# Performance work log

Hardware: AMD Instinct MI355X
Metric: run time of the kernel (lower is better)

## Reference

```python
import jax, jax.numpy as jnp
import numpy as np

NUM_CONN = 8

def _ein_reduce(f):
    # Einstein t-norm fold over last axis: T(a,b) = ab / (2 - (a+b-ab))
    acc = f[..., 0]
    for i in range(1, f.shape[-1]):
        b = f[..., i]
        ab = acc * b
        acc = ab / (2.0 - (acc + b - ab))
    return acc

def _coein_reduce(f):
    # Einstein t-conorm fold over last axis: S(a,b) = (a+b) / (1 + ab)
    acc = f[..., 0]
    for i in range(1, f.shape[-1]):
        b = f[..., i]
        acc = (acc + b) / (1.0 + acc * b)
    return acc

def _ddlg_layer(x, w, idx, is_train):
    # x: [B, in], idx: [out, C] int, w: [out, 4]
    feats = x[:, idx]                      # [B, out, C] gather
    ops = jnp.stack([
        jnp.min(feats, axis=-1),
        jnp.max(feats, axis=-1),
        _ein_reduce(feats),
        _coein_reduce(feats),
    ], axis=-1)                            # [B, out, 4]
    if is_train:
        prob = jax.nn.softmax(w, axis=-1)  # [out, 4]
    else:
        prob = jax.nn.one_hot(jnp.argmax(w, axis=-1), 4, dtype=x.dtype)
    return jnp.einsum('bof,of->bo', ops, prob)

def setup_inputs() -> dict:
    key = jax.random.key(0)
    ks = jax.random.split(key, 6)
    sizes = [4096, 2048, 1024, 2048, 4096]
    x = jax.random.uniform(ks[0], (4096, sizes[0]), dtype=jnp.float32)
    ws = [jax.random.normal(ks[1 + i], (sizes[i + 1], 4), dtype=jnp.float32) for i in range(4)]
    rng = np.random.default_rng(0)
    idxs = []
    for i in range(4):
        # randperm-without-replacement per output neuron
        perm = np.argsort(rng.random((sizes[i + 1], sizes[i])), axis=-1)[:, :NUM_CONN]
        idxs.append(jnp.asarray(perm, dtype=jnp.int32))
    return {
        'x': x,
        'w0': ws[0], 'w1': ws[1], 'w2': ws[2], 'w3': ws[3],
        'idx0': idxs[0], 'idx1': idxs[1], 'idx2': idxs[2], 'idx3': idxs[3],
        'is_train': 1,
    }

def reference(x, w0, w1, w2, w3, idx0, idx1, idx2, idx3, is_train):
    h = _ddlg_layer(x, w0, idx0, is_train)
    h = _ddlg_layer(h, w1, idx1, is_train)
    h = _ddlg_layer(h, w2, idx2, is_train)
    h = _ddlg_layer(h, w3, idx3, is_train)
    return h
```

## Files before the change

kernel.cpp:

```cpp
#include <hip/hip_runtime.h>


#define BATCH 4096

typedef _Float16 h4 __attribute__((ext_vector_type(4)));

__device__ __forceinline__ float fastrcp(float x) { return __builtin_amdgcn_rcpf(x); }
__device__ __forceinline__ _Float16 hrcp(_Float16 x) {
#if __has_builtin(__builtin_amdgcn_rcph)
    return __builtin_amdgcn_rcph(x);
#else
    return (_Float16)__builtin_amdgcn_rcpf((float)x);
#endif
}
__device__ __forceinline__ h4 splat(_Float16 s) { h4 v = {s, s, s, s}; return v; }

__global__ __launch_bounds__(256) void prep_k(const float* __restrict__ w0,
                                              const float* __restrict__ w1,
                                              const float* __restrict__ w2,
                                              const float* __restrict__ w3,
                                              const int* __restrict__ is_train,
                                              h4* __restrict__ probsH) {
    const int g = blockIdx.x * 256 + threadIdx.x;
    const float* w; int o;
    if (g < 2048)      { w = w0; o = g; }
    else if (g < 3072) { w = w1; o = g - 2048; }
    else if (g < 5120) { w = w2; o = g - 3072; }
    else               { w = w3; o = g - 5120; }
    float wv[4];
#pragma unroll
    for (int c = 0; c < 4; ++c) wv[c] = w[(o << 2) + c];
    float p[4];
    if (*is_train) {
        float m = fmaxf(fmaxf(wv[0], wv[1]), fmaxf(wv[2], wv[3]));
        float s = 0.0f;
#pragma unroll
        for (int c = 0; c < 4; ++c) { p[c] = __expf(wv[c] - m); s += p[c]; }
        float inv = fastrcp(s);
#pragma unroll
        for (int c = 0; c < 4; ++c) p[c] *= inv;
    } else {
        int a = 0; float best = wv[0];
#pragma unroll
        for (int c = 1; c < 4; ++c) if (wv[c] > best) { best = wv[c]; a = c; }
#pragma unroll
        for (int c = 0; c < 4; ++c) p[c] = (c == a) ? 1.0f : 0.0f;
    }
    probsH[g] = h4{(_Float16)p[0], (_Float16)p[1], (_Float16)p[2], (_Float16)p[3]};
}

struct Chain { h4 mn, mx, De, Ne, Nc, Dc; };

__device__ __forceinline__ void chain_init(Chain& C, h4 v, h4 one, h4 two) {
    C.mn = v; C.mx = v; C.De = v;
    C.Ne = two - v; C.Nc = one + v; C.Dc = one - v;
}
__device__ __forceinline__ void chain_step(Chain& C, h4 v, h4 two) {
    C.mn = __builtin_elementwise_min(C.mn, v);
    C.mx = __builtin_elementwise_max(C.mx, v);
    C.De *= v;
    C.Ne *= (two - v);
    C.Nc += C.Nc * v;
    C.Dc -= C.Dc * v;
}
__device__ __forceinline__ h4 finale(const Chain& C, h4 P) {
    h4 s1 = C.Ne + C.De;
    h4 s2 = C.Nc + C.Dc;
    h4 d1 = C.Nc - C.Dc;
    h4 ss = s1 * s2;
    h4 r;
#pragma unroll
    for (int e = 0; e < 4; ++e) r[e] = hrcp(ss[e]);
    h4 t1 = (C.De + C.De) * s2;
    h4 t2 = d1 * s1;
    h4 num = splat(P[2]) * t1 + splat(P[3]) * t2;
    return splat(P[0]) * C.mn + splat(P[1]) * C.mx + num * r;
}

__device__ __forceinline__ h4 gate1(const h4* __restrict__ rows,
                                    const int4* __restrict__ idx,
                                    const h4* __restrict__ probs, int o) {
    const int4 i0 = idx[o * 2], i1 = idx[o * 2 + 1];
    const h4 P = probs[o];
    h4 A[8];
    A[0] = rows[i0.x]; A[1] = rows[i0.y]; A[2] = rows[i0.z]; A[3] = rows[i0.w];
    A[4] = rows[i1.x]; A[5] = rows[i1.y]; A[6] = rows[i1.z]; A[7] = rows[i1.w];
    const h4 one = splat((_Float16)1.0f), two = splat((_Float16)2.0f);
    Chain C; chain_init(C, A[0], one, two);
#pragma unroll
    for (int c = 1; c < 8; ++c) chain_step(C, A[c], two);
    return finale(C, P);
}

__device__ __forceinline__ void gate2(const h4* __restrict__ rows,
                                      const int4* __restrict__ idx,
                                      const h4* __restrict__ probs,
                                      int o0, h4& ra, h4& rb) {
    const int4 a0 = idx[o0 * 2],     a1 = idx[o0 * 2 + 1];
    const int4 b0 = idx[o0 * 2 + 2], b1 = idx[o0 * 2 + 3];
    const h4 PA = probs[o0], PB = probs[o0 + 1];
    h4 A[8], B[8];
    A[0] = rows[a0.x]; A[1] = rows[a0.y]; A[2] = rows[a0.z]; A[3] = rows[a0.w];
    A[4] = rows[a1.x]; A[5] = rows[a1.y]; A[6] = rows[a1.z]; A[7] = rows[a1.w];
    B[0] = rows[b0.x]; B[1] = rows[b0.y]; B[2] = rows[b0.z]; B[3] = rows[b0.w];
    B[4] = rows[b1.x]; B[5] = rows[b1.y]; B[6] = rows[b1.z]; B[7] = rows[b1.w];
    const h4 one = splat((_Float16)1.0f), two = splat((_Float16)2.0f);
    Chain CA, CB;
    chain_init(CA, A[0], one, two);
    chain_init(CB, B[0], one, two);
#pragma unroll
    for (int c = 1; c < 8; ++c) {
        chain_step(CA, A[c], two);
        chain_step(CB, B[c], two);
    }
    ra = finale(CA, PA);
    rb = finale(CB, PB);
}

struct alignas(16) H4x2 { h4 a, b; };

__global__ __launch_bounds__(1024, 8) void ddlg_fused(const float* __restrict__ x,
                                                      const h4* __restrict__ probsH,
                                                      const int4* __restrict__ idx0,
                                                      const int4* __restrict__ idx1,
                                                      const int4* __restrict__ idx2,
                                                      const int4* __restrict__ idx3,
                                                      float* __restrict__ out) {
    __shared__ __align__(16) _Float16 lds[24576];
    const int t  = threadIdx.x;
    const int b0 = blockIdx.x << 2;

    const h4* xl  = (const h4*)lds;
    const h4* h0v = (const h4*)(lds + 16384);
    const h4* h1v = (const h4*)lds;
    const h4* h2v = (const h4*)(lds + 16384);

#pragma unroll
    for (int c = 0; c < 4; ++c) {
        const int j = (c << 10) + t;
        const float v0 = x[(size_t)(b0 + 0) * 4096 + j];
        const float v1 = x[(size_t)(b0 + 1) * 4096 + j];
        const float v2 = x[(size_t)(b0 + 2) * 4096 + j];
        const float v3 = x[(size_t)(b0 + 3) * 4096 + j];
        h4 hv;
        hv[0] = (_Float16)v0; hv[1] = (_Float16)v1;
        hv[2] = (_Float16)v2; hv[3] = (_Float16)v3;
        *(h4*)(lds + (j << 2)) = hv;
    }
    __syncthreads();

    {
        h4 ra, rb;
        gate2(xl, idx0, probsH, 2 * t, ra, rb);
        *(H4x2*)(lds + 16384 + (t << 3)) = H4x2{ra, rb};
    }
    __syncthreads();

    {
        h4 r = gate1(h0v, idx1, probsH + 2048, t);
        *(h4*)(lds + (t << 2)) = r;
    }
    __syncthreads();

    {
        h4 ra, rb;
        gate2(h1v, idx2, probsH + 3072, 2 * t, ra, rb);
        *(H4x2*)(lds + 16384 + (t << 3)) = H4x2{ra, rb};
    }
    __syncthreads();

    {
        h4 r0, r1, r2, r3;
        gate2(h2v, idx3, probsH + 5120, 4 * t,     r0, r1);
        gate2(h2v, idx3, probsH + 5120, 4 * t + 2, r2, r3);
#pragma unroll
        for (int b = 0; b < 4; ++b) {
            float4 o4 = make_float4((float)r0[b], (float)r1[b],
                                    (float)r2[b], (float)r3[b]);
            *(float4*)(out + (size_t)(b0 + b) * 4096 + (t << 2)) = o4;
        }
    }
}

extern "C" void kernel_launch(void* const* d_in, const int* in_sizes, int n_in,
                              void* d_out, int out_size, void* d_ws, size_t ws_size,
                              hipStream_t stream) {
    const float* x        = (const float*)d_in[0];
    const float* w0       = (const float*)d_in[1];
    const float* w1       = (const float*)d_in[2];
    const float* w2       = (const float*)d_in[3];
    const float* w3       = (const float*)d_in[4];
    const int4*  idx0     = (const int4*)d_in[5];
    const int4*  idx1     = (const int4*)d_in[6];
    const int4*  idx2     = (const int4*)d_in[7];
    const int4*  idx3     = (const int4*)d_in[8];
    const int*   is_train = (const int*)d_in[9];
    float*       out      = (float*)d_out;

    h4* probsH = (h4*)d_ws;

    prep_k<<<36, 256, 0, stream>>>(w0, w1, w2, w3, is_train, probsH);
    ddlg_fused<<<1024, 1024, 0, stream>>>(x, probsH, idx0, idx1, idx2, idx3, out);
}
```

Measured before the change: 164.2 us.

## Process eight batch rows per block with 16-byte LDS gathers

Each block now handles 8 batch rows instead of 4, storing activations as 8 packed halves (uint4) per feature in LDS. One gathered 16-byte LDS read now serves 8 batch elements, halving index and probability loads per output and amortising gather address work. The cost is twice the LDS per block (96 KB), fewer resident blocks per CU (launch bound lowered to 4), more live registers per thread, and half as many blocks in the grid.

```diff
diff --git a/kernel.cpp b/kernel.cpp
--- a/kernel.cpp
+++ b/kernel.cpp
@@ -3,6 +3,7 @@
 
 #define BATCH 4096
 
+typedef _Float16 h2 __attribute__((ext_vector_type(2)));
 typedef _Float16 h4 __attribute__((ext_vector_type(4)));
 
 __device__ __forceinline__ float fastrcp(float x) { return __builtin_amdgcn_rcpf(x); }
@@ -13,7 +14,7 @@
     return (_Float16)__builtin_amdgcn_rcpf((float)x);
 #endif
 }
-__device__ __forceinline__ h4 splat(_Float16 s) { h4 v = {s, s, s, s}; return v; }
+__device__ __forceinline__ h2 splat2(_Float16 s) { h2 v = {s, s}; return v; }
 
 __global__ __launch_bounds__(256) void prep_k(const float* __restrict__ w0,
                                               const float* __restrict__ w1,
@@ -49,134 +50,145 @@
     probsH[g] = h4{(_Float16)p[0], (_Float16)p[1], (_Float16)p[2], (_Float16)p[3]};
 }
 
-struct Chain { h4 mn, mx, De, Ne, Nc, Dc; };
-
-__device__ __forceinline__ void chain_init(Chain& C, h4 v, h4 one, h4 two) {
-    C.mn = v; C.mx = v; C.De = v;
-    C.Ne = two - v; C.Nc = one + v; C.Dc = one - v;
-}
-__device__ __forceinline__ void chain_step(Chain& C, h4 v, h4 two) {
-    C.mn = __builtin_elementwise_min(C.mn, v);
-    C.mx = __builtin_elementwise_max(C.mx, v);
-    C.De *= v;
-    C.Ne *= (two - v);
-    C.Nc += C.Nc * v;
-    C.Dc -= C.Dc * v;
-}
-__device__ __forceinline__ h4 finale(const Chain& C, h4 P) {
-    h4 s1 = C.Ne + C.De;
-    h4 s2 = C.Nc + C.Dc;
-    h4 d1 = C.Nc - C.Dc;
-    h4 ss = s1 * s2;
-    h4 r;
-#pragma unroll
-    for (int e = 0; e < 4; ++e) r[e] = hrcp(ss[e]);
-    h4 t1 = (C.De + C.De) * s2;
-    h4 t2 = d1 * s1;
-    h4 num = splat(P[2]) * t1 + splat(P[3]) * t2;
-    return splat(P[0]) * C.mn + splat(P[1]) * C.mx + num * r;
-}
-
-__device__ __forceinline__ h4 gate1(const h4* __restrict__ rows,
-                                    const int4* __restrict__ idx,
-                                    const h4* __restrict__ probs, int o) {
+struct Raw8 { h2 q[4]; };
+
+__device__ __forceinline__ Raw8 row_at(const uint4* __restrict__ rows, int i) {
+    const uint4 v = rows[i];
+    Raw8 r;
+    r.q[0] = __builtin_bit_cast(h2, v.x);
+    r.q[1] = __builtin_bit_cast(h2, v.y);
+    r.q[2] = __builtin_bit_cast(h2, v.z);
+    r.q[3] = __builtin_bit_cast(h2, v.w);
+    return r;
+}
+__device__ __forceinline__ uint4 raw_bits(Raw8 r) {
+    return uint4{__builtin_bit_cast(unsigned, r.q[0]), __builtin_bit_cast(unsigned, r.q[1]),
+                 __builtin_bit_cast(unsigned, r.q[2]), __builtin_bit_cast(unsigned, r.q[3])};
+}
+
+struct Chain8 { h2 mn[4], mx[4], De[4], Ne[4], Nc[4], Dc[4]; };
+
+__device__ __forceinline__ void cinit(Chain8& C, Raw8 v) {
+    const h2 one = splat2((_Float16)1.0f), two = splat2((_Float16)2.0f);
+#pragma unroll
+    for (int q = 0; q < 4; ++q) {
+        C.mn[q] = v.q[q]; C.mx[q] = v.q[q]; C.De[q] = v.q[q];
+        C.Ne[q] = two - v.q[q];
+        C.Nc[q] = one + v.q[q];
+        C.Dc[q] = one - v.q[q];
+    }
+}
+__device__ __forceinline__ void cstep(Chain8& C, Raw8 v) {
+    const h2 two = splat2((_Float16)2.0f);
+#pragma unroll
+    for (int q = 0; q < 4; ++q) {
+        C.mn[q] = __builtin_elementwise_min(C.mn[q], v.q[q]);
+        C.mx[q] = __builtin_elementwise_max(C.mx[q], v.q[q]);
+        C.De[q] *= v.q[q];
+        C.Ne[q] *= (two - v.q[q]);
+        C.Nc[q] += C.Nc[q] * v.q[q];
+        C.Dc[q] -= C.Dc[q] * v.q[q];
+    }
+}
+__device__ __forceinline__ Raw8 finale(const Chain8& C, h4 P) {
+    const h2 P0 = splat2(P[0]), P1 = splat2(P[1]);
+    const h2 P2 = splat2(P[2]), P3 = splat2(P[3]);
+    Raw8 res;
+#pragma unroll
+    for (int q = 0; q < 4; ++q) {
+        h2 s1 = C.Ne[q] + C.De[q];
+        h2 s2 = C.Nc[q] + C.Dc[q];
+        h2 d1 = C.Nc[q] - C.Dc[q];
+        h2 ss = s1 * s2;
+        h2 r  = {hrcp(ss[0]), hrcp(ss[1])};
+        h2 t1 = (C.De[q] + C.De[q]) * s2;
+        h2 t2 = d1 * s1;
+        h2 num = P2 * t1 + P3 * t2;
+        res.q[q] = P0 * C.mn[q] + P1 * C.mx[q] + num * r;
+    }
+    return res;
+}
+
+__device__ __forceinline__ Raw8 gate8(const uint4* __restrict__ rows,
+                                      const int4* __restrict__ idx,
+                                      const h4* __restrict__ probs, int o) {
     const int4 i0 = idx[o * 2], i1 = idx[o * 2 + 1];
     const h4 P = probs[o];
-    h4 A[8];
-    A[0] = rows[i0.x]; A[1] = rows[i0.y]; A[2] = rows[i0.z]; A[3] = rows[i0.w];
-    A[4] = rows[i1.x]; A[5] = rows[i1.y]; A[6] = rows[i1.z]; A[7] = rows[i1.w];
-    const h4 one = splat((_Float16)1.0f), two = splat((_Float16)2.0f);
-    Chain C; chain_init(C, A[0], one, two);
-#pragma unroll
-    for (int c = 1; c < 8; ++c) chain_step(C, A[c], two);
+    Raw8 A[8];
+    A[0] = row_at(rows, i0.x); A[1] = row_at(rows, i0.y);
+    A[2] = row_at(rows, i0.z); A[3] = row_at(rows, i0.w);
+    A[4] = row_at(rows, i1.x); A[5] = row_at(rows, i1.y);
+    A[6] = row_at(rows, i1.z); A[7] = row_at(rows, i1.w);
+    Chain8 C; cinit(C, A[0]);
+#pragma unroll
+    for (int c = 1; c < 8; ++c) cstep(C, A[c]);
     return finale(C, P);
 }
 
-__device__ __forceinline__ void gate2(const h4* __restrict__ rows,
-                                      const int4* __restrict__ idx,
-                                      const h4* __restrict__ probs,
-                                      int o0, h4& ra, h4& rb) {
-    const int4 a0 = idx[o0 * 2],     a1 = idx[o0 * 2 + 1];
-    const int4 b0 = idx[o0 * 2 + 2], b1 = idx[o0 * 2 + 3];
-    const h4 PA = probs[o0], PB = probs[o0 + 1];
-    h4 A[8], B[8];
-    A[0] = rows[a0.x]; A[1] = rows[a0.y]; A[2] = rows[a0.z]; A[3] = rows[a0.w];
-    A[4] = rows[a1.x]; A[5] = rows[a1.y]; A[6] = rows[a1.z]; A[7] = rows[a1.w];
-    B[0] = rows[b0.x]; B[1] = rows[b0.y]; B[2] = rows[b0.z]; B[3] = rows[b0.w];
-    B[4] = rows[b1.x]; B[5] = rows[b1.y]; B[6] = rows[b1.z]; B[7] = rows[b1.w];
-    const h4 one = splat((_Float16)1.0f), two = splat((_Float16)2.0f);
-    Chain CA, CB;
-    chain_init(CA, A[0], one, two);
-    chain_init(CB, B[0], one, two);
-#pragma unroll
-    for (int c = 1; c < 8; ++c) {
-        chain_step(CA, A[c], two);
-        chain_step(CB, B[c], two);
-    }
-    ra = finale(CA, PA);
-    rb = finale(CB, PB);
-}
-
-struct alignas(16) H4x2 { h4 a, b; };
-
-__global__ __launch_bounds__(1024, 8) void ddlg_fused(const float* __restrict__ x,
+__global__ __launch_bounds__(1024, 4) void ddlg_fused(const float* __restrict__ x,
                                                       const h4* __restrict__ probsH,
                                                       const int4* __restrict__ idx0,
                                                       const int4* __restrict__ idx1,
                                                       const int4* __restrict__ idx2,
                                                       const int4* __restrict__ idx3,
                                                       float* __restrict__ out) {
-    __shared__ __align__(16) _Float16 lds[24576];
+    __shared__ __align__(16) _Float16 lds[49152];
     const int t  = threadIdx.x;
-    const int b0 = blockIdx.x << 2;
-
-    const h4* xl  = (const h4*)lds;
-    const h4* h0v = (const h4*)(lds + 16384);
-    const h4* h1v = (const h4*)lds;
-    const h4* h2v = (const h4*)(lds + 16384);
+    const int b0 = blockIdx.x << 3;
+
+    const uint4* xv  = (const uint4*)lds;
+    const uint4* h0v = (const uint4*)(lds + 32768);
+    const uint4* h1v = (const uint4*)lds;
+    const uint4* h2v = (const uint4*)(lds + 32768);
 
 #pragma unroll
     for (int c = 0; c < 4; ++c) {
         const int j = (c << 10) + t;
-        const float v0 = x[(size_t)(b0 + 0) * 4096 + j];
-        const float v1 = x[(size_t)(b0 + 1) * 4096 + j];
-        const float v2 = x[(size_t)(b0 + 2) * 4096 + j];
-        const float v3 = x[(size_t)(b0 + 3) * 4096 + j];
-        h4 hv;
-        hv[0] = (_Float16)v0; hv[1] = (_Float16)v1;
-        hv[2] = (_Float16)v2; hv[3] = (_Float16)v3;
-        *(h4*)(lds + (j << 2)) = hv;
-    }
-    __syncthreads();
-
-    {
-        h4 ra, rb;
-        gate2(xl, idx0, probsH, 2 * t, ra, rb);
-        *(H4x2*)(lds + 16384 + (t << 3)) = H4x2{ra, rb};
-    }
-    __syncthreads();
-
-    {
-        h4 r = gate1(h0v, idx1, probsH + 2048, t);
-        *(h4*)(lds + (t << 2)) = r;
-    }
-    __syncthreads();
-
-    {
-        h4 ra, rb;
-        gate2(h1v, idx2, probsH + 3072, 2 * t, ra, rb);
-        *(H4x2*)(lds + 16384 + (t << 3)) = H4x2{ra, rb};
-    }
-    __syncthreads();
-
-    {
-        h4 r0, r1, r2, r3;
-        gate2(h2v, idx3, probsH + 5120, 4 * t,     r0, r1);
-        gate2(h2v, idx3, probsH + 5120, 4 * t + 2, r2, r3);
-#pragma unroll
-        for (int b = 0; b < 4; ++b) {
-            float4 o4 = make_float4((float)r0[b], (float)r1[b],
-                                    (float)r2[b], (float)r3[b]);
+        h2 p[4];
+#pragma unroll
+        for (int qq = 0; qq < 4; ++qq) {
+            const float va = x[(size_t)(b0 + 2 * qq + 0) * 4096 + j];
+            const float vb = x[(size_t)(b0 + 2 * qq + 1) * 4096 + j];
+            p[qq] = h2{(_Float16)va, (_Float16)vb};
+        }
+        uint4 hv = {__builtin_bit_cast(unsigned, p[0]), __builtin_bit_cast(unsigned, p[1]),
+                    __builtin_bit_cast(unsigned, p[2]), __builtin_bit_cast(unsigned, p[3])};
+        *(uint4*)(lds + (j << 3)) = hv;
+    }
+    __syncthreads();
+
+    {
+        Raw8 ra = gate8(xv, idx0, probsH, 2 * t);
+        Raw8 rb = gate8(xv, idx0, probsH, 2 * t + 1);
+        *(uint4*)(lds + 32768 + (t << 4))     = raw_bits(ra);
+        *(uint4*)(lds + 32768 + (t << 4) + 8) = raw_bits(rb);
+    }
+    __syncthreads();
+
+    {
+        Raw8 r = gate8(h0v, idx1, probsH + 2048, t);
+        *(uint4*)(lds + (t << 3)) = raw_bits(r);
+    }
+    __syncthreads();
+
+    {
+        Raw8 ra = gate8(h1v, idx2, probsH + 3072, 2 * t);
+        Raw8 rb = gate8(h1v, idx2, probsH + 3072, 2 * t + 1);
+        *(uint4*)(lds + 32768 + (t << 4))     = raw_bits(ra);
+        *(uint4*)(lds + 32768 + (t << 4) + 8) = raw_bits(rb);
+    }
+    __syncthreads();
+
+    {
+        Raw8 r0 = gate8(h2v, idx3, probsH + 5120, 4 * t);
+        Raw8 r1 = gate8(h2v, idx3, probsH + 5120, 4 * t + 1);
+        Raw8 r2 = gate8(h2v, idx3, probsH + 5120, 4 * t + 2);
+        Raw8 r3 = gate8(h2v, idx3, probsH + 5120, 4 * t + 3);
+#pragma unroll
+        for (int b = 0; b < 8; ++b) {
+            const int q = b >> 1, e = b & 1;
+            float4 o4 = make_float4((float)r0.q[q][e], (float)r1.q[q][e],
+                                    (float)r2.q[q][e], (float)r3.q[q][e]);
             *(float4*)(out + (size_t)(b0 + b) * 4096 + (t << 2)) = o4;
         }
     }
@@ -200,5 +212,5 @@
     h4* probsH = (h4*)d_ws;
 
     prep_k<<<36, 256, 0, stream>>>(w0, w1, w2, w3, is_train, probsH);
-    ddlg_fused<<<1024, 1024, 0, stream>>>(x, probsH, idx0, idx1, idx2, idx3, out);
-}
+    ddlg_fused<<<512, 1024, 0, stream>>>(x, probsH, idx0, idx1, idx2, idx3, out);
+}
```

Measured after the change: 170.8 us. 4.0% more time.

## Process two batch rows per block with 512 threads and packed half2

Applied to the files above, without the earlier changes.

Each block now handles 2 batch rows instead of 4, using 512 threads and 24KB of LDS instead of 1024 threads and 48KB. Activations are stored as packed half2 words and each thread loops over several output neurons per layer. The aim is higher occupancy and smaller blocks with shorter barrier stalls. In exchange, the index and probability loads are amortised over half as many batch rows, and the final output is written as scalar floats instead of float4.

```diff
diff --git a/kernel.cpp b/kernel.cpp
--- a/kernel.cpp
+++ b/kernel.cpp
@@ -1,8 +1,7 @@
 #include <hip/hip_runtime.h>
 
 
-#define BATCH 4096
-
+typedef _Float16 h2 __attribute__((ext_vector_type(2)));
 typedef _Float16 h4 __attribute__((ext_vector_type(4)));
 
 __device__ __forceinline__ float fastrcp(float x) { return __builtin_amdgcn_rcpf(x); }
@@ -13,7 +12,11 @@
     return (_Float16)__builtin_amdgcn_rcpf((float)x);
 #endif
 }
-__device__ __forceinline__ h4 splat(_Float16 s) { h4 v = {s, s, s, s}; return v; }
+__device__ __forceinline__ h2 splat2(_Float16 s) { h2 v = {s, s}; return v; }
+__device__ __forceinline__ unsigned packh2(float a, float b) {
+    h2 v = {(_Float16)a, (_Float16)b};
+    return __builtin_bit_cast(unsigned, v);
+}
 
 __global__ __launch_bounds__(256) void prep_k(const float* __restrict__ w0,
                                               const float* __restrict__ w1,
@@ -49,13 +52,18 @@
     probsH[g] = h4{(_Float16)p[0], (_Float16)p[1], (_Float16)p[2], (_Float16)p[3]};
 }
 
-struct Chain { h4 mn, mx, De, Ne, Nc, Dc; };
+struct Chain { h2 mn, mx, De, Ne, Nc, Dc; };
 
-__device__ __forceinline__ void chain_init(Chain& C, h4 v, h4 one, h4 two) {
+__device__ __forceinline__ h2 row_at(const unsigned* __restrict__ rows, int i) {
+    return __builtin_bit_cast(h2, rows[i]);
+}
+__device__ __forceinline__ void cinit(Chain& C, h2 v) {
+    const h2 one = splat2((_Float16)1.0f), two = splat2((_Float16)2.0f);
     C.mn = v; C.mx = v; C.De = v;
     C.Ne = two - v; C.Nc = one + v; C.Dc = one - v;
 }
-__device__ __forceinline__ void chain_step(Chain& C, h4 v, h4 two) {
+__device__ __forceinline__ void cstep(Chain& C, h2 v) {
+    const h2 two = splat2((_Float16)2.0f);
     C.mn = __builtin_elementwise_min(C.mn, v);
     C.mx = __builtin_elementwise_max(C.mx, v);
     C.De *= v;
@@ -63,122 +71,89 @@
     C.Nc += C.Nc * v;
     C.Dc -= C.Dc * v;
 }
-__device__ __forceinline__ h4 finale(const Chain& C, h4 P) {
-    h4 s1 = C.Ne + C.De;
-    h4 s2 = C.Nc + C.Dc;
-    h4 d1 = C.Nc - C.Dc;
-    h4 ss = s1 * s2;
-    h4 r;
-#pragma unroll
-    for (int e = 0; e < 4; ++e) r[e] = hrcp(ss[e]);
-    h4 t1 = (C.De + C.De) * s2;
-    h4 t2 = d1 * s1;
-    h4 num = splat(P[2]) * t1 + splat(P[3]) * t2;
-    return splat(P[0]) * C.mn + splat(P[1]) * C.mx + num * r;
+__device__ __forceinline__ h2 finale(const Chain& C, h4 P) {
+    h2 s1 = C.Ne + C.De;
+    h2 s2 = C.Nc + C.Dc;
+    h2 d1 = C.Nc - C.Dc;
+    h2 ss = s1 * s2;
+    h2 r  = {hrcp(ss[0]), hrcp(ss[1])};
+    h2 t1 = (C.De + C.De) * s2;
+    h2 t2 = d1 * s1;
+    h2 num = splat2(P[2]) * t1 + splat2(P[3]) * t2;
+    return splat2(P[0]) * C.mn + splat2(P[1]) * C.mx + num * r;
 }
 
-__device__ __forceinline__ h4 gate1(const h4* __restrict__ rows,
-                                    const int4* __restrict__ idx,
-                                    const h4* __restrict__ probs, int o) {
+__device__ __forceinline__ h2 gate(const unsigned* __restrict__ rows,
+                                   const int4* __restrict__ idx,
+                                   const h4* __restrict__ probs, int o) {
     const int4 i0 = idx[o * 2], i1 = idx[o * 2 + 1];
     const h4 P = probs[o];
-    h4 A[8];
-    A[0] = rows[i0.x]; A[1] = rows[i0.y]; A[2] = rows[i0.z]; A[3] = rows[i0.w];
-    A[4] = rows[i1.x]; A[5] = rows[i1.y]; A[6] = rows[i1.z]; A[7] = rows[i1.w];
-    const h4 one = splat((_Float16)1.0f), two = splat((_Float16)2.0f);
-    Chain C; chain_init(C, A[0], one, two);
+    h2 A[8];
+    A[0] = row_at(rows, i0.x); A[1] = row_at(rows, i0.y);
+    A[2] = row_at(rows, i0.z); A[3] = row_at(rows, i0.w);
+    A[4] = row_at(rows, i1.x); A[5] = row_at(rows, i1.y);
+    A[6] = row_at(rows, i1.z); A[7] = row_at(rows, i1.w);
+    Chain C; cinit(C, A[0]);
 #pragma unroll
-    for (int c = 1; c < 8; ++c) chain_step(C, A[c], two);
+    for (int c = 1; c < 8; ++c) cstep(C, A[c]);
     return finale(C, P);
 }
 
-__device__ __forceinline__ void gate2(const h4* __restrict__ rows,
-                                      const int4* __restrict__ idx,
-                                      const h4* __restrict__ probs,
-                                      int o0, h4& ra, h4& rb) {
-    const int4 a0 = idx[o0 * 2],     a1 = idx[o0 * 2 + 1];
-    const int4 b0 = idx[o0 * 2 + 2], b1 = idx[o0 * 2 + 3];
-    const h4 PA = probs[o0], PB = probs[o0 + 1];
-    h4 A[8], B[8];
-    A[0] = rows[a0.x]; A[1] = rows[a0.y]; A[2] = rows[a0.z]; A[3] = rows[a0.w];
-    A[4] = rows[a1.x]; A[5] = rows[a1.y]; A[6] = rows[a1.z]; A[7] = rows[a1.w];
-    B[0] = rows[b0.x]; B[1] = rows[b0.y]; B[2] = rows[b0.z]; B[3] = rows[b0.w];
-    B[4] = rows[b1.x]; B[5] = rows[b1.y]; B[6] = rows[b1.z]; B[7] = rows[b1.w];
-    const h4 one = splat((_Float16)1.0f), two = splat((_Float16)2.0f);
-    Chain CA, CB;
-    chain_init(CA, A[0], one, two);
-    chain_init(CB, B[0], one, two);
-#pragma unroll
-    for (int c = 1; c < 8; ++c) {
-        chain_step(CA, A[c], two);
-        chain_step(CB, B[c], two);
-    }
-    ra = finale(CA, PA);
-    rb = finale(CB, PB);
-}
+__global__ __launch_bounds__(512, 8) void ddlg_fused(const float* __restrict__ x,
+                                                     const h4* __restrict__ probsH,
+                                                     const int4* __restrict__ idx0,
+                                                     const int4* __restrict__ idx1,
+                                                     const int4* __restrict__ idx2,
+                                                     const int4* __restrict__ idx3,
+                                                     float* __restrict__ out) {
+    __shared__ __align__(16) unsigned lds[6144];
+    const int t  = threadIdx.x;
+    const int b0 = blockIdx.x << 1;
 
-struct alignas(16) H4x2 { h4 a, b; };
-
-__global__ __launch_bounds__(1024, 8) void ddlg_fused(const float* __restrict__ x,
-                                                      const h4* __restrict__ probsH,
-                                                      const int4* __restrict__ idx0,
-                                                      const int4* __restrict__ idx1,
-                                                      const int4* __restrict__ idx2,
-                                                      const int4* __restrict__ idx3,
-                                                      float* __restrict__ out) {
-    __shared__ __align__(16) _Float16 lds[24576];
-    const int t  = threadIdx.x;
-    const int b0 = blockIdx.x << 2;
-
-    const h4* xl  = (const h4*)lds;
-    const h4* h0v = (const h4*)(lds + 16384);
-    const h4* h1v = (const h4*)lds;
-    const h4* h2v = (const h4*)(lds + 16384);
+    const unsigned* xl  = lds;
+    const unsigned* h0v = lds + 4096;
+    const unsigned* h1v = lds;
+    const unsigned* h2v = lds + 4096;
 
 #pragma unroll
-    for (int c = 0; c < 4; ++c) {
-        const int j = (c << 10) + t;
+    for (int c = 0; c < 8; ++c) {
+        const int j = (c << 9) + t;
         const float v0 = x[(size_t)(b0 + 0) * 4096 + j];
         const float v1 = x[(size_t)(b0 + 1) * 4096 + j];
-        const float v2 = x[(size_t)(b0 + 2) * 4096 + j];
-        const float v3 = x[(size_t)(b0 + 3) * 4096 + j];
-        h4 hv;
-        hv[0] = (_Float16)v0; hv[1] = (_Float16)v1;
-        hv[2] = (_Float16)v2; hv[3] = (_Float16)v3;
-        *(h4*)(lds + (j << 2)) = hv;
+        lds[j] = packh2(v0, v1);
     }
     __syncthreads();
 
-    {
-        h4 ra, rb;
-        gate2(xl, idx0, probsH, 2 * t, ra, rb);
-        *(H4x2*)(lds + 16384 + (t << 3)) = H4x2{ra, rb};
+#pragma unroll
+    for (int k = 0; k < 4; ++k) {
+        const int o = (k << 9) + t;
+        h2 r = gate(xl, idx0, probsH, o);
+        lds[4096 + o] = __builtin_bit_cast(unsigned, r);
     }
     __syncthreads();
 
-    {
-        h4 r = gate1(h0v, idx1, probsH + 2048, t);
-        *(h4*)(lds + (t << 2)) = r;
+#pragma unroll
+    for (int k = 0; k < 2; ++k) {
+        const int o = (k << 9) + t;
+        h2 r = gate(h0v, idx1, probsH + 2048, o);
+        lds[o] = __builtin_bit_cast(unsigned, r);
     }
     __syncthreads();
 
-    {
-        h4 ra, rb;
-        gate2(h1v, idx2, probsH + 3072, 2 * t, ra, rb);
-        *(H4x2*)(lds + 16384 + (t << 3)) = H4x2{ra, rb};
+#pragma unroll
+    for (int k = 0; k < 4; ++k) {
+        const int o = (k << 9) + t;
+        h2 r = gate(h1v, idx2, probsH + 3072, o);
+        lds[4096 + o] = __builtin_bit_cast(unsigned, r);
     }
     __syncthreads();
 
-    {
-        h4 r0, r1, r2, r3;
-        gate2(h2v, idx3, probsH + 5120, 4 * t,     r0, r1);
-        gate2(h2v, idx3, probsH + 5120, 4 * t + 2, r2, r3);
 #pragma unroll
-        for (int b = 0; b < 4; ++b) {
-            float4 o4 = make_float4((float)r0[b], (float)r1[b],
-                                    (float)r2[b], (float)r3[b]);
-            *(float4*)(out + (size_t)(b0 + b) * 4096 + (t << 2)) = o4;
-        }
+    for (int k = 0; k < 8; ++k) {
+        const int o = (k << 9) + t;
+        h2 r = gate(h2v, idx3, probsH + 5120, o);
+        out[(size_t)(b0 + 0) * 4096 + o] = (float)r[0];
+        out[(size_t)(b0 + 1) * 4096 + o] = (float)r[1];
     }
 }
 
@@ -200,5 +175,5 @@
     h4* probsH = (h4*)d_ws;
 
     prep_k<<<36, 256, 0, stream>>>(w0, w1, w2, w3, is_train, probsH);
-    ddlg_fused<<<1024, 1024, 0, stream>>>(x, probsH, idx0, idx1, idx2, idx3, out);
+    ddlg_fused<<<2048, 512, 0, stream>>>(x, probsH, idx0, idx1, idx2, idx3, out);
 }
```

Result: no change. 167.2 us (+1.9%).
